# Kernel tuning notes

Measured on AMD Instinct MI355X. Metric: run time of the kernel, lower is better.

The kernel has to match this reference:

```python
import jax, jax.numpy as jnp
import numpy as np

E = 512   # embed_size == hidden_size (required: step-0 'embed' is the init output of size hidden)
H = 512
A = 512   # attention dim
V = 20000
P = 196
B = 128
T = 24


def setup_inputs() -> dict:
    key = jax.random.key(0)
    ks = jax.random.split(key, 20)
    s = 0.02
    return {
        "features": jax.random.normal(ks[0], (B, P, E), jnp.float32),
        "captions": jax.random.randint(ks[1], (B, T), 0, V),
        "emb": jax.random.normal(ks[2], (V, E), jnp.float32) * s,
        "W_init_h": jax.random.normal(ks[3], (E, H), jnp.float32) * s,
        "b_init_h": jnp.zeros((H,), jnp.float32),
        "W_init_o": jax.random.normal(ks[4], (E, H), jnp.float32) * s,
        "b_init_o": jnp.zeros((H,), jnp.float32),
        "Wf": jax.random.normal(ks[5], (E, A), jnp.float32) * s,
        "bf": jnp.zeros((A,), jnp.float32),
        "Wh": jax.random.normal(ks[6], (H, A), jnp.float32) * s,
        "bh": jnp.zeros((A,), jnp.float32),
        "v_att": jax.random.normal(ks[7], (A,), jnp.float32) * s,
        "W_ih": jax.random.normal(ks[8], (3 * H, 2 * E), jnp.float32) * s,
        "W_hh": jax.random.normal(ks[9], (3 * H, H), jnp.float32) * s,
        "b_ih": jnp.zeros((3 * H,), jnp.float32),
        "b_hh": jnp.zeros((3 * H,), jnp.float32),
        "W_out": jax.random.normal(ks[10], (V, H), jnp.float32) * s,
        "b_out": jnp.zeros((V,), jnp.float32),
    }


def reference(features, emb, W_init_h, b_init_h, W_init_o, b_init_o,
              Wf, bf, Wh, bh, v_att, W_ih, W_hh, b_ih, b_hh,
              W_out, b_out, captions):
    # init_hidden_state
    avg = features.mean(axis=1)                          # [B,E]
    hidden0 = jnp.tanh(avg @ W_init_h + b_init_h)        # [B,H]
    output0 = jnp.tanh(avg @ W_init_o + b_init_o)        # [B,H]

    emb_caps = emb[captions]                             # [B,T,E]
    # teacher forcing: step 0 uses init output, step i>0 uses embeddings[:, i-1]
    embed_seq = jnp.concatenate([output0[:, None, :], emb_caps[:, :-1, :]], axis=1)
    xs = embed_seq.transpose(1, 0, 2)                    # [T,B,E]

    feat_proj = features @ Wf + bf                       # [B,P,A] (precompute attn key proj)

    def step(h, x_emb):
        # additive attention over pixels
        score = jnp.tanh(feat_proj + (h @ Wh + bh)[:, None, :]) @ v_att   # [B,P]
        alpha = jax.nn.softmax(score, axis=1)
        ctx = jnp.einsum('bp,bpe->be', alpha, features)                   # [B,E]
        x = jnp.concatenate([x_emb, ctx], axis=1)                         # [B,2E]
        # single-step GRU (PyTorch gate order r,z,n)
        gi = x @ W_ih.T + b_ih
        gh = h @ W_hh.T + b_hh
        gi_r, gi_z, gi_n = jnp.split(gi, 3, axis=1)
        gh_r, gh_z, gh_n = jnp.split(gh, 3, axis=1)
        r = jax.nn.sigmoid(gi_r + gh_r)
        z = jax.nn.sigmoid(gi_z + gh_z)
        n = jnp.tanh(gi_n + r * gh_n)
        h_new = (1.0 - z) * n + z * h
        pred = h_new @ W_out.T + b_out                                    # [B,V]
        return h_new, pred

    _, preds = jax.lax.scan(step, hidden0, xs)           # preds: [T,B,V]
    return preds.transpose(1, 0, 2)                      # [B,T,V]
```

## Files before the change

kernel.cpp:

```cpp
#include <hip/hip_runtime.h>

#define Bb 128
#define Tt 24
#define Ee 512
#define Hh 512
#define Aa 512
#define Vv 20000
#define Pp 196
#define TV (Tt*Vv)
#define NBLK 512
#define NTHR 256
#define GT (NBLK*NTHR)
#define SMEM_BYTES 34816

typedef __attribute__((ext_vector_type(8))) short bfrag;
typedef __attribute__((ext_vector_type(4))) float f4;
typedef __attribute__((ext_vector_type(4))) unsigned short us4;

#define MFMA16(a,b,c) __builtin_amdgcn_mfma_f32_16x16x32_bf16(a,b,c,0,0,0)

__device__ __forceinline__ unsigned short f2bf(float f){
  unsigned int x = __builtin_bit_cast(unsigned int, f);
  x += 0x7fffu + ((x >> 16) & 1u);
  return (unsigned short)(x >> 16);
}
__device__ __forceinline__ float bfu2f(unsigned short u){
  unsigned int x = ((unsigned int)u) << 16;
  return __builtin_bit_cast(float, x);
}
#define LOG2E 1.442695041f
__device__ __forceinline__ float fexp2(float x){ return __builtin_amdgcn_exp2f(x); }
__device__ __forceinline__ float frcp (float x){ return __builtin_amdgcn_rcpf(x); }
__device__ __forceinline__ float tanh_f(float x){ return 1.0f - 2.0f*frcp(1.0f + fexp2((2.0f*LOG2E)*x)); }
__device__ __forceinline__ float sigm_f(float x){ return frcp(1.0f + fexp2(-LOG2E*x)); }

__device__ __forceinline__ unsigned long long scld8(const void* p){
  return __hip_atomic_load((const unsigned long long*)p, __ATOMIC_RELAXED, __HIP_MEMORY_SCOPE_AGENT);
}
__device__ __forceinline__ unsigned scld4(const unsigned* p){
  return __hip_atomic_load(p, __ATOMIC_RELAXED, __HIP_MEMORY_SCOPE_AGENT);
}
__device__ __forceinline__ void scst4(unsigned* p, unsigned v){
  __hip_atomic_store(p, v, __ATOMIC_RELAXED, __HIP_MEMORY_SCOPE_AGENT);
}
__device__ __forceinline__ void scstf(float* p, float v){
  __hip_atomic_store(p, v, __ATOMIC_RELAXED, __HIP_MEMORY_SCOPE_AGENT);
}

__device__ __forceinline__ void set_flag(unsigned* line, unsigned v){
  asm volatile("s_waitcnt vmcnt(0)" ::: "memory");
  __syncthreads();
  if(threadIdx.x == 0) scst4(line, v);
}
__device__ __forceinline__ void poll_flags(const unsigned* base, int n, unsigned tgt){
  int tid = threadIdx.x;
  for(;;){
    int ok = (tid < n) ? (scld4(base + tid*16) >= tgt) : 1;
    if(__syncthreads_count(ok) == NTHR) break;
    __builtin_amdgcn_s_sleep(4);
  }
  asm volatile("" ::: "memory");
}

__device__ __forceinline__ void gbar2(unsigned* sync, unsigned phase){
  __syncthreads();
  int tid = threadIdx.x, blk = blockIdx.x;
  if(tid == 0)
    (void)__hip_atomic_fetch_add(sync + (blk & 31)*16, 1u,
                                 __ATOMIC_RELEASE, __HIP_MEMORY_SCOPE_AGENT);
  if(blk == 0){
    for(;;){
      int ok = (tid < 32) ? (scld4(sync + tid*16) >= phase*16u) : 1;
      if(__syncthreads_count(ok) == NTHR) break;
      __builtin_amdgcn_s_sleep(2);
    }
    if(tid == 0) scst4(sync + 32*16, phase);
  }
  if(tid == 0){
    while(scld4(sync + 32*16) < phase) __builtin_amdgcn_s_sleep(2);
    (void)__hip_atomic_load(sync + 32*16, __ATOMIC_ACQUIRE, __HIP_MEMORY_SCOPE_AGENT);
  }
  __syncthreads();
}

__global__ void k_zero(unsigned* s){
  int i = blockIdx.x*256 + threadIdx.x;
  s[i] = 0u;
}

__device__ __forceinline__ void cast_loop(const float* __restrict__ s,
                                          unsigned short* __restrict__ d,
                                          int n4, int gtid){
  for(int i = gtid; i < n4; i += GT){
    float4 v = ((const float4*)s)[i];
    us4 o; o[0]=f2bf(v.x); o[1]=f2bf(v.y); o[2]=f2bf(v.z); o[3]=f2bf(v.w);
    ((us4*)d)[i] = o;
  }
}
__device__ __forceinline__ void tr_tile(const float* __restrict__ S,
                                        unsigned short* __restrict__ D,
                                        int it, int jt, int tid, float (*T)[33]){
  int er = tid>>3, c4 = (tid&7)*4;
  float4 v = *(const float4*)(S + (size_t)(jt*32+er)*512 + it*32 + c4);
  T[er][c4+0]=v.x; T[er][c4+1]=v.y; T[er][c4+2]=v.z; T[er][c4+3]=v.w;
  __syncthreads();
  us4 o;
  o[0]=f2bf(T[c4+0][er]); o[1]=f2bf(T[c4+1][er]);
  o[2]=f2bf(T[c4+2][er]); o[3]=f2bf(T[c4+3][er]);
  *(us4*)(D + (size_t)(it*32+er)*512 + jt*32 + c4) = o;
  __syncthreads();
}

__device__ __forceinline__ void stage16(char* dstSM, const unsigned short* src, int R0){
  int tid = threadIdx.x;
  #pragma unroll
  for(int j=0;j<8;j++){
    int u = tid + j*256;
    int row = u >> 7, c8 = u & 127;
    unsigned long long q = scld8(src + (size_t)(R0+row)*Hh + c8*4);
    int bo = (row<<10) + (c8<<3);
    bo ^= (row&7)<<4;
    *(unsigned long long*)(dstSM + bo) = q;
  }
}


__device__ void attention_task(int b, const float* __restrict__ hpr_t,
                               const unsigned short* __restrict__ fpb,
                               const unsigned short* __restrict__ featsB,
                               const float* __restrict__ vatt,
                               unsigned short* __restrict__ ctx_t, char* SM)
{
  float* hp  = (float*)SM;
  float* vp  = hp + 512;
  float* sc  = vp + 512;
  float* red = sc + 200;
  int tid = threadIdx.x;
  {
    unsigned long long q = scld8(hpr_t + (size_t)b*Aa + tid*2);
    float2 hv = __builtin_bit_cast(float2, q);
    float2 vv = *(const float2*)(vatt + tid*2);
    int a0 = tid*2, a1 = a0+1;
    hp[((a0&31)<<4)+(a0>>5)] = hv.x;
    hp[((a1&31)<<4)+(a1>>5)] = hv.y;
    vp[((a0&31)<<4)+(a0>>5)] = vv.x;
    vp[((a1&31)<<4)+(a1>>5)] = vv.y;
  }
  __syncthreads();
  int grp = tid >> 4, gl = tid & 15;
  for(int pass=0; pass<13; pass++){
    int p = pass*16 + grp;
    float acc = 0.0f;
    if(p < Pp){
      const unsigned short* fr = fpb + ((size_t)b*Pp + p)*Aa + gl*32;
      #pragma unroll
      for(int j=0;j<32;j+=8){
        bfrag fv = *(const bfrag*)(fr + j);
        #pragma unroll
        for(int q=0;q<8;q++){
          int idx = ((j+q)<<4) + gl;
          float x = bfu2f((unsigned short)fv[q]) + hp[idx];
          acc += tanh_f(x) * vp[idx];
        }
      }
    }
    acc += __shfl_xor(acc, 1, 64);
    acc += __shfl_xor(acc, 2, 64);
    acc += __shfl_xor(acc, 4, 64);
    acc += __shfl_xor(acc, 8, 64);
    if(p < Pp && gl == 0) sc[p] = acc;
  }
  __syncthreads();
  if(tid < 64){
    float m = -1e30f;
    for(int i=0;i<4;i++){ int p = tid + i*64; if(p < Pp) m = fmaxf(m, sc[p]); }
    for(int off=1; off<64; off<<=1) m = fmaxf(m, __shfl_xor(m, off, 64));
    float s = 0.0f;
    for(int i=0;i<4;i++){ int p = tid + i*64; if(p < Pp) s += fexp2((sc[p]-m)*LOG2E); }
    for(int off=1; off<64; off<<=1) s += __shfl_xor(s, off, 64);
    if(tid == 0){ red[0] = m; red[1] = frcp(s); }
  }
  __syncthreads();
  float mx = red[0], rS = red[1];
  float al_t = 0.0f;
  if(tid < Pp) al_t = fexp2((sc[tid]-mx)*LOG2E) * rS;
  __syncthreads();
  if(tid < Pp) sc[tid] = al_t;
  __syncthreads();
  float c0 = 0.f, c1 = 0.f;
  const unsigned int* fb = (const unsigned int*)(featsB + (size_t)b*Pp*Ee);
  for(int p=0;p<Pp;p++){
    float al = sc[p];
    unsigned int u = fb[(size_t)p*256 + tid];
    unsigned int lo = (u & 0xffffu) << 16, hi = u & 0xffff0000u;
    c0 += al * __builtin_bit_cast(float, lo);
    c1 += al * __builtin_bit_cast(float, hi);
  }
  unsigned int cw = ((unsigned int)f2bf(c1) << 16) | (unsigned int)f2bf(c0);
  scst4((unsigned*)ctx_t + (size_t)b*256 + tid, cw);
}

__device__ void hproj_mfma(int R0, int HC0, const char* SMh,
                           const unsigned short* __restrict__ WhT,
                           const float* __restrict__ bhv, float* __restrict__ hpr)
{
  int tid = threadIdx.x;
  int w = tid>>6, l = tid&63, l16 = l&15, lk = l>>4;
  int a = HC0 + w*16 + l16;
  f4 acc = (f4)(0.0f);
  for(int k0=0;k0<512;k0+=32){
    int koff = k0 + lk*8;
    int bo = (l16<<10) + (koff<<1); bo ^= (l16&7)<<4;
    bfrag ah = *(const bfrag*)(SMh + bo);
    bfrag bq = *(const bfrag*)(WhT + (size_t)a*Hh + koff);
    acc = MFMA16(ah, bq, acc);
  }
  float bias = bhv[a];
  #pragma unroll
  for(int i=0;i<4;i++){
    int row = lk*4 + i;
    scstf(hpr + (size_t)(R0+row)*Aa + a, acc[i] + bias);
  }
}

__device__ void gates_phaseA(int R0, int HC0, const unsigned short* __restrict__ eseqT,
                             const unsigned short* __restrict__ WihB,
                             const unsigned short* __restrict__ WhhB,
                             const char* SMh, f4 (&agh)[3], f4 (&agi)[3])
{
  int tid = threadIdx.x;
  int w = tid>>6, l = tid&63, l16 = l&15, lk = l>>4;
  int hcol = HC0 + w*16 + l16;
  #pragma unroll
  for(int q=0;q<3;q++){ agh[q]=(f4)(0.f); agi[q]=(f4)(0.f); }
  for(int k0=0;k0<512;k0+=32){
    int koff = k0 + lk*8;
    int bo = (l16<<10) + (koff<<1); bo ^= (l16&7)<<4;
    bfrag ah = *(const bfrag*)(SMh + bo);
    bfrag ae = *(const bfrag*)(eseqT + (size_t)(R0+l16)*Ee + koff);
    #pragma unroll
    for(int q=0;q<3;q++){
      int j = q*512 + hcol;
      bfrag bh_ = *(const bfrag*)(WhhB + (size_t)j*512  + koff);
      bfrag be  = *(const bfrag*)(WihB + (size_t)j*1024 + koff);
      agh[q] = MFMA16(ah, bh_, agh[q]);
      agi[q] = MFMA16(ae, be,  agi[q]);
    }
  }
}

__device__ void gates_phaseB(int R0, int HC0, const char* SMc,
                             const unsigned short* __restrict__ WihB,
                             const float* __restrict__ bih, const float* __restrict__ bhh,
                             const float* __restrict__ hf_cur, float* __restrict__ hf_nxt,
                             unsigned short* __restrict__ hbU_nxt,
                             f4 (&agh)[3], f4 (&agi)[3], char* SM_HB)
{
  int tid = threadIdx.x;
  int w = tid>>6, l = tid&63, l16 = l&15, lk = l>>4;
  int hcol = HC0 + w*16 + l16;
  for(int k0=0;k0<512;k0+=32){
    int koff = k0 + lk*8;
    int bo = (l16<<10) + (koff<<1); bo ^= (l16&7)<<4;
    bfrag ac = *(const bfrag*)(SMc + bo);
    #pragma unroll
    for(int q=0;q<3;q++){
      int j = q*512 + hcol;
      bfrag bc = *(const bfrag*)(WihB + (size_t)j*1024 + 512 + koff);
      agi[q] = MFMA16(ac, bc, agi[q]);
    }
  }
  float bir = bih[hcol],      bhr = bhh[hcol];
  float biz = bih[512+hcol],  bhz = bhh[512+hcol];
  float bin = bih[1024+hcol], bhn = bhh[1024+hcol];
  unsigned short (*HB)[64] = (unsigned short(*)[64])SM_HB;
  #pragma unroll
  for(int i=0;i<4;i++){
    int row = lk*4 + i;
    int b = R0 + row;
    float r_ = sigm_f(agi[0][i] + bir + agh[0][i] + bhr);
    float z_ = sigm_f(agi[1][i] + biz + agh[1][i] + bhz);
    float n_ = tanh_f(agi[2][i] + bin + r_*(agh[2][i] + bhn));
    float ho = hf_cur[(size_t)b*Hh + hcol];
    float hn = (1.0f - z_)*n_ + z_*ho;
    hf_nxt[(size_t)b*Hh + hcol] = hn;
    HB[row][w*16 + l16] = f2bf(hn);
  }
  __syncthreads();
  #pragma unroll
  for(int j=0;j<2;j++){
    int widx = tid + j*256;
    int row = widx >> 5, pr = widx & 31;
    unsigned uu = (unsigned)HB[row][pr*2] | ((unsigned)HB[row][pr*2+1] << 16);
    scst4((unsigned*)(hbU_nxt + (size_t)(R0+row)*Hh + HC0) + pr, uu);
  }
}

__device__ void pred_task32(int pt, int tw, const unsigned short* __restrict__ hb_cur,
                            const unsigned short* __restrict__ WoutB,
                            const float* __restrict__ bout, float* __restrict__ out,
                            char* SM)
{
  int tid = threadIdx.x;
  int vchunk = pt >> 2, mbase = (pt & 3)*32;
  #pragma unroll
  for(int j=0;j<16;j++){
    int u = tid + j*256;
    int row = u >> 7, c8 = u & 127;
    unsigned long long q = scld8(hb_cur + (size_t)(mbase+row)*Hh + c8*4);
    int bo = (row<<10) + (c8<<3);
    bo ^= (row&7)<<4;
    *(unsigned long long*)(SM + bo) = q;
  }
  __syncthreads();
  int w = tid>>6, l = tid&63, l16 = l&15, lk = l>>4;
  int nb = vchunk*256 + w*64;
  f4 acc[2][4];
  #pragma unroll
  for(int mi=0;mi<2;mi++) for(int ni=0;ni<4;ni++) acc[mi][ni] = (f4)(0.0f);
  for(int k0=0;k0<512;k0+=32){
    int koff = k0 + lk*8;
    bfrag af[2], bq[4];
    #pragma unroll
    for(int mi=0;mi<2;mi++){
      int row = mi*16 + l16;
      int bo = (row<<10) + (koff<<1);
      bo ^= (row&7)<<4;
      af[mi] = *(const bfrag*)(SM + bo);
    }
    #pragma unroll
    for(int ni=0;ni<4;ni++){
      int v = nb + ni*16 + l16; if(v > Vv-1) v = Vv-1;
      bq[ni] = *(const bfrag*)(WoutB + (size_t)v*Hh + koff);
    }
    #pragma unroll
    for(int mi=0;mi<2;mi++)
      #pragma unroll
      for(int ni=0;ni<4;ni++)
        acc[mi][ni] = MFMA16(af[mi], bq[ni], acc[mi][ni]);
  }
  #pragma unroll
  for(int ni=0;ni<4;ni++){
    int v = nb + ni*16 + l16;
    if(v < Vv){
      float bias = bout[v];
      #pragma unroll
      for(int mi=0;mi<2;mi++){
        #pragma unroll
        for(int i=0;i<4;i++){
          int br = mbase + mi*16 + lk*4 + i;
          __builtin_nontemporal_store(acc[mi][ni][i] + bias,
              out + (size_t)br*TV + (size_t)tw*Vv + v);
        }
      }
    }
  }
  __syncthreads();
}

__global__ __launch_bounds__(NTHR, 4) void k_all(
    const float* feats, const int* caps, const float* emb,
    const float* Winh, const float* binh, const float* Wino, const float* bino,
    const float* Wf, const float* bfv, const float* Wh, const float* bhv,
    const float* vatt, const float* Wih, const float* Whh,
    const float* bih, const float* bhh, const float* Wout, const float* bout,
    float* out,
    float* hfR, unsigned short* hbU, float* hpr,
    unsigned short* ctxR, unsigned short* avgB, unsigned short* eseq,
    unsigned short* WfT, unsigned short* WhT,
    unsigned short* WinhT, unsigned short* WinoT,
    unsigned short* WihB, unsigned short* WhhB,
    unsigned short* fpb, unsigned short* featsB, unsigned short* WoutB,
    unsigned* sync)
{
  extern __shared__ char SMEM[];
  const int blk = blockIdx.x, tid = threadIdx.x;
  const int gtid = blk*NTHR + tid;
  unsigned* flagsA = sync + 40*16;
  unsigned* flagsG = sync + 168*16;
  unsigned* flagsP = sync + 240*16;
  unsigned* aggP   = sync + 304*16;
  float* h_f0 = hfR;
  unsigned short* h_b0 = hbU;

  cast_loop(Wih,  WihB,  (3*Hh*2*Ee)/4, gtid);
  cast_loop(Whh,  WhhB,  (3*Hh*Hh)/4,   gtid);
  cast_loop(Wout, WoutB, (Vv*Hh)/4,     gtid);
  cast_loop(feats,featsB,(Bb*Pp*Ee)/4,  gtid);
  for(int task = blk; task < 1024; task += NBLK){
    int z = task >> 8, rt = task & 255;
    int it = rt & 15, jt = rt >> 4;
    const float* S = (z==0)?Wf:(z==1)?Wh:(z==2)?Winh:Wino;
    unsigned short* D = (z==0)?WfT:(z==1)?WhT:(z==2)?WinhT:WinoT;
    tr_tile(S, D, it, jt, tid, (float(*)[33])SMEM);
  }
  if(blk < Bb){
    int b = blk;
    const float* fb = feats + (size_t)b*Pp*Ee;
    float a0=0.f, a1=0.f;
    for(int p=0;p<Pp;p++){
      float2 v = *(const float2*)(fb + (size_t)p*Ee + tid*2);
      a0 += v.x; a1 += v.y;
    }
    a0 *= (1.0f/Pp); a1 *= (1.0f/Pp);
    unsigned int pack = ((unsigned int)f2bf(a1)<<16) | (unsigned int)f2bf(a0);
    ((unsigned int*)avgB)[(size_t)b*256 + tid] = pack;
  }
  for(int task = blk; task < (Tt-1)*Bb; task += NBLK){
    int ts = task/Bb + 1, b = task%Bb;
    int cap = caps[b*Tt + (ts-1)];
    float2 v = *(const float2*)(emb + (size_t)cap*Ee + tid*2);
    unsigned int pack = ((unsigned int)f2bf(v.y)<<16) | (unsigned int)f2bf(v.x);
    ((unsigned int*)(eseq + ((size_t)ts*Bb + b)*Ee))[tid] = pack;
  }
  gbar2(sync, 1);

  for(int task = blk; task < 1584; task += NBLK){
    int w = tid>>6, l = tid&63, l16 = l&15, lk = l>>4;
    if(task < 1568){
      int bx = task % 196, by = task / 196;
      size_t m_base = (size_t)bx*128 + (w&1)*64;
      int nb = by*64 + (w>>1)*32;
      f4 acc[4][2];
      #pragma unroll
      for(int mi=0;mi<4;mi++) for(int ni=0;ni<2;ni++) acc[mi][ni] = (f4)(0.0f);
      for(int k0=0;k0<512;k0+=32){
        int koff = k0 + lk*8;
        bfrag af[4], bq[2];
        #pragma unroll
        for(int mi=0;mi<4;mi++) af[mi] = *(const bfrag*)(featsB + (m_base+mi*16+l16)*512 + koff);
        #pragma unroll
        for(int ni=0;ni<2;ni++) bq[ni] = *(const bfrag*)(WfT + (size_t)(nb+ni*16+l16)*512 + koff);
        #pragma unroll
        for(int mi=0;mi<4;mi++)
          #pragma unroll
          for(int ni=0;ni<2;ni++)
            acc[mi][ni] = MFMA16(af[mi], bq[ni], acc[mi][ni]);
      }
      #pragma unroll
      for(int ni=0;ni<2;ni++){
        int a = nb + ni*16 + l16;
        float bias = bfv[a];
        #pragma unroll
        for(int mi=0;mi<4;mi++){
          size_t r = m_base + mi*16 + lk*4;
          #pragma unroll
          for(int i=0;i<4;i++)
            fpb[(r+i)*512 + a] = f2bf(acc[mi][ni][i] + bias);
        }
      }
    } else {
      int idx = task - 1568;
      int y = idx >> 3, xb = idx & 7;
      int m0 = (w&1)*64, nb = xb*64 + (w>>1)*32;
      const unsigned short* Wt = y ? WinoT : WinhT;
      const float* bias = y ? bino : binh;
      f4 acc[4][2];
      #pragma unroll
      for(int mi=0;mi<4;mi++) for(int ni=0;ni<2;ni++) acc[mi][ni] = (f4)(0.0f);
      for(int k0=0;k0<512;k0+=32){
        int koff = k0 + lk*8;
        bfrag af[4], bq[2];
        #pragma unroll
        for(int mi=0;mi<4;mi++) af[mi] = *(const bfrag*)(avgB + (size_t)(m0+mi*16+l16)*512 + koff);
        #pragma unroll
        for(int ni=0;ni<2;ni++) bq[ni] = *(const bfrag*)(Wt + (size_t)(nb+ni*16+l16)*512 + koff);
        #pragma unroll
        for(int mi=0;mi<4;mi++)
          #pragma unroll
          for(int ni=0;ni<2;ni++)
            acc[mi][ni] = MFMA16(af[mi], bq[ni], acc[mi][ni]);
      }
      #pragma unroll
      for(int ni=0;ni<2;ni++){
        int n = nb + ni*16 + l16;
        float bv = bias[n];
        #pragma unroll
        for(int mi=0;mi<4;mi++){
          int bb = m0 + mi*16 + lk*4;
          #pragma unroll
          for(int i=0;i<4;i++){
            float val = tanh_f(acc[mi][ni][i] + bv);
            if(y==0){ h_f0[(size_t)(bb+i)*Hh + n] = val; h_b0[(size_t)(bb+i)*Hh + n] = f2bf(val); }
            else    { eseq[(size_t)(bb+i)*Ee + n] = f2bf(val); }
          }
        }
      }
    }
  }
  gbar2(sync, 2);

  int xcd = blk & 7, slot = blk >> 3;

  if(slot < 16){
    int b = slot*8 + xcd;
    int rg = b >> 4;
    for(int t=0; t<Tt; t++){
      poll_flags(flagsP + rg*8*16, 8, (unsigned)(t+1));
      attention_task(b, hpr + (size_t)(t&1)*Bb*Aa, fpb, featsB, vatt,
                     ctxR + (size_t)(t&3)*Bb*Ee, SMEM);
      set_flag(flagsA + b*16, (unsigned)(t+1));
    }
  } else if(slot < 24){
    int r = slot - 16, c = xcd;
    int R0 = r*16, HC0 = c*64;
    char* SMh = SMEM;
    char* SMc = SMEM + 16384;
    char* SMB = SMEM + 32768;
    f4 agh[3], agi[3];
    stage16(SMh, hbU, R0);
    __syncthreads();
    hproj_mfma(R0, HC0, SMh, WhT, bhv, hpr);
    set_flag(flagsP + (r*8+c)*16, 1u);
    gates_phaseA(R0, HC0, eseq, WihB, WhhB, SMh, agh, agi);
    for(int t=0; t<Tt; t++){
      poll_flags(flagsA + R0*16, 16, (unsigned)(t+1));
      stage16(SMc, ctxR + (size_t)(t&3)*Bb*Ee, R0);
      __syncthreads();
      gates_phaseB(R0, HC0, SMc, WihB, bih, bhh,
                   hfR + (size_t)(t&1)*Bb*Hh, hfR + (size_t)((t+1)&1)*Bb*Hh,
                   hbU + (size_t)(t+1)*Bb*Hh, agh, agi, SMB);
      set_flag(flagsG + (r*8+c)*16, (unsigned)(t+1));
      if(t+1 < Tt){
        poll_flags(flagsG + r*8*16, 8, (unsigned)(t+1));
        stage16(SMh, hbU + (size_t)(t+1)*Bb*Hh, R0);
        __syncthreads();
        hproj_mfma(R0, HC0, SMh, WhT, bhv, hpr + (size_t)((t+1)&1)*Bb*Aa);
        set_flag(flagsP + (r*8+c)*16, (unsigned)(t+2));
        gates_phaseA(R0, HC0, eseq + (size_t)(t+1)*Bb*Ee, WihB, WhhB, SMh, agh, agi);
      }
    }
  } else {
    int ps = slot - 24;
    int pt = xcd*40 + ps;
    if(ps == 0){
      for(int t=1; t<=Tt; t++){
        poll_flags(flagsG, 64, (unsigned)t);
        if(tid == 0) scst4(aggP + xcd*16, (unsigned)t);
        pred_task32(pt, t-1, hbU + (size_t)t*Bb*Hh, WoutB, bout, out, SMEM);
      }
    } else if(pt < 316){
      for(int t=1; t<=Tt; t++){
        poll_flags(aggP + xcd*16, 1, (unsigned)t);
        pred_task32(pt, t-1, hbU + (size_t)t*Bb*Hh, WoutB, bout, out, SMEM);
      }
    }
  }
}

extern "C" void kernel_launch(void* const* d_in, const int* in_sizes, int n_in,
                              void* d_out, int out_size, void* d_ws, size_t ws_size,
                              hipStream_t stream)
{
  const float* feats = (const float*)d_in[0];
  const int*   caps  = (const int*)d_in[1];
  const float* emb   = (const float*)d_in[2];
  const float* Winh  = (const float*)d_in[3];
  const float* binh  = (const float*)d_in[4];
  const float* Wino  = (const float*)d_in[5];
  const float* bino  = (const float*)d_in[6];
  const float* Wf    = (const float*)d_in[7];
  const float* bfv   = (const float*)d_in[8];
  const float* Wh    = (const float*)d_in[9];
  const float* bhv   = (const float*)d_in[10];
  const float* vatt  = (const float*)d_in[11];
  const float* Wih   = (const float*)d_in[12];
  const float* Whh   = (const float*)d_in[13];
  const float* bih   = (const float*)d_in[14];
  const float* bhh   = (const float*)d_in[15];
  const float* Wout  = (const float*)d_in[16];
  const float* bout  = (const float*)d_in[17];
  float* out = (float*)d_out;

  char* ws = (char*)d_ws;
  size_t off = 0;
  auto alloc = [&](size_t bytes){
    off = (off + 255) & ~(size_t)255;
    void* p = ws + off; off += bytes; return p;
  };
  unsigned* syncp = (unsigned*)alloc(32768);
  float* hfR = (float*)alloc((size_t)2*Bb*Hh*4);
  unsigned short* hbU = (unsigned short*)alloc((size_t)(Tt+1)*Bb*Hh*2);
  float* hpr = (float*)alloc((size_t)2*Bb*Aa*4);
  unsigned short* ctxR  = (unsigned short*)alloc((size_t)4*Bb*Ee*2);
  unsigned short* avgB  = (unsigned short*)alloc((size_t)Bb*Ee*2);
  unsigned short* eseq  = (unsigned short*)alloc((size_t)Tt*Bb*Ee*2);
  unsigned short* WfT   = (unsigned short*)alloc((size_t)Ee*Aa*2);
  unsigned short* WhT   = (unsigned short*)alloc((size_t)Hh*Aa*2);
  unsigned short* WinhT = (unsigned short*)alloc((size_t)Ee*Hh*2);
  unsigned short* WinoT = (unsigned short*)alloc((size_t)Ee*Hh*2);
  unsigned short* WihB  = (unsigned short*)alloc((size_t)3*Hh*2*Ee*2);
  unsigned short* WhhB  = (unsigned short*)alloc((size_t)3*Hh*Hh*2);
  unsigned short* fpb   = (unsigned short*)alloc((size_t)Bb*Pp*Aa*2);
  unsigned short* featsB= (unsigned short*)alloc((size_t)Bb*Pp*Ee*2);
  unsigned short* WoutB = (unsigned short*)alloc((size_t)Vv*Hh*2);
  if(ws_size < off) return;

  k_zero<<<32, 256, 0, stream>>>(syncp);
  k_all<<<NBLK, NTHR, SMEM_BYTES, stream>>>(
      feats, caps, emb, Winh, binh, Wino, bino, Wf, bfv, Wh, bhv, vatt,
      Wih, Whh, bih, bhh, Wout, bout, out,
      hfR, hbU, hpr, ctxR, avgB, eseq,
      WfT, WhT, WinhT, WinoT, WihB, WhhB, fpb, featsB, WoutB, syncp);
}
```

Baseline: 1.445 ms.

## Batch output projection over two timesteps to reuse W_out loads

The prediction blocks now wait for two consecutive hidden states and run the vocabulary projection for both together, so each W_out fragment loaded from memory feeds twice as many MFMAs. Shared memory grows to 64KB and launch bounds drop to 2 blocks per CU to fit the second staged hidden tile. The gate scratch buffer is padded to a stride of 88, the context loop is unrolled, and the poll sleep is shortened. In exchange, predictions lag the recurrence by an extra step, and the lower occupancy bound may raise register use or limit co-residency of the 512 persistent blocks.

Measured after the change: 1.448 ms. About the same (+0.2%).

```diff
diff --git a/kernel.cpp b/kernel.cpp
--- a/kernel.cpp
+++ b/kernel.cpp
@@ -11,7 +11,7 @@
 #define NBLK 512
 #define NTHR 256
 #define GT (NBLK*NTHR)
-#define SMEM_BYTES 34816
+#define SMEM_BYTES 65536
 
 typedef __attribute__((ext_vector_type(8))) short bfrag;
 typedef __attribute__((ext_vector_type(4))) float f4;
@@ -57,7 +57,7 @@
   for(;;){
     int ok = (tid < n) ? (scld4(base + tid*16) >= tgt) : 1;
     if(__syncthreads_count(ok) == NTHR) break;
-    __builtin_amdgcn_s_sleep(4);
+    __builtin_amdgcn_s_sleep(2);
   }
   asm volatile("" ::: "memory");
 }
@@ -189,6 +189,7 @@
   __syncthreads();
   float c0 = 0.f, c1 = 0.f;
   const unsigned int* fb = (const unsigned int*)(featsB + (size_t)b*Pp*Ee);
+  #pragma unroll 4
   for(int p=0;p<Pp;p++){
     float al = sc[p];
     unsigned int u = fb[(size_t)p*256 + tid];
@@ -240,9 +241,9 @@
     bfrag ae = *(const bfrag*)(eseqT + (size_t)(R0+l16)*Ee + koff);
     #pragma unroll
     for(int q=0;q<3;q++){
-      int j = q*512 + hcol;
-      bfrag bh_ = *(const bfrag*)(WhhB + (size_t)j*512  + koff);
-      bfrag be  = *(const bfrag*)(WihB + (size_t)j*1024 + koff);
+      int jj = q*512 + hcol;
+      bfrag bh_ = *(const bfrag*)(WhhB + (size_t)jj*512  + koff);
+      bfrag be  = *(const bfrag*)(WihB + (size_t)jj*1024 + koff);
       agh[q] = MFMA16(ah, bh_, agh[q]);
       agi[q] = MFMA16(ae, be,  agi[q]);
     }
@@ -254,7 +255,7 @@
                              const float* __restrict__ bih, const float* __restrict__ bhh,
                              const float* __restrict__ hf_cur, float* __restrict__ hf_nxt,
                              unsigned short* __restrict__ hbU_nxt,
-                             f4 (&agh)[3], f4 (&agi)[3], char* SM_HB)
+                             f4 (&agh)[3], f4 (&agi)[3], unsigned short* HBp)
 {
   int tid = threadIdx.x;
   int w = tid>>6, l = tid&63, l16 = l&15, lk = l>>4;
@@ -265,15 +266,14 @@
     bfrag ac = *(const bfrag*)(SMc + bo);
     #pragma unroll
     for(int q=0;q<3;q++){
-      int j = q*512 + hcol;
-      bfrag bc = *(const bfrag*)(WihB + (size_t)j*1024 + 512 + koff);
+      int jj = q*512 + hcol;
+      bfrag bc = *(const bfrag*)(WihB + (size_t)jj*1024 + 512 + koff);
       agi[q] = MFMA16(ac, bc, agi[q]);
     }
   }
   float bir = bih[hcol],      bhr = bhh[hcol];
   float biz = bih[512+hcol],  bhz = bhh[512+hcol];
   float bin = bih[1024+hcol], bhn = bhh[1024+hcol];
-  unsigned short (*HB)[64] = (unsigned short(*)[64])SM_HB;
   #pragma unroll
   for(int i=0;i<4;i++){
     int row = lk*4 + i;
@@ -284,22 +284,24 @@
     float ho = hf_cur[(size_t)b*Hh + hcol];
     float hn = (1.0f - z_)*n_ + z_*ho;
     hf_nxt[(size_t)b*Hh + hcol] = hn;
-    HB[row][w*16 + l16] = f2bf(hn);
+    HBp[row*88 + w*16 + l16] = f2bf(hn);
   }
   __syncthreads();
   #pragma unroll
   for(int j=0;j<2;j++){
     int widx = tid + j*256;
     int row = widx >> 5, pr = widx & 31;
-    unsigned uu = (unsigned)HB[row][pr*2] | ((unsigned)HB[row][pr*2+1] << 16);
+    unsigned uu = (unsigned)HBp[row*88 + pr*2] | ((unsigned)HBp[row*88 + pr*2+1] << 16);
     scst4((unsigned*)(hbU_nxt + (size_t)(R0+row)*Hh + HC0) + pr, uu);
   }
 }
 
-__device__ void pred_task32(int pt, int tw, const unsigned short* __restrict__ hb_cur,
-                            const unsigned short* __restrict__ WoutB,
-                            const float* __restrict__ bout, float* __restrict__ out,
-                            char* SM)
+__device__ void pred_pair(int pt, int twA,
+                          const unsigned short* __restrict__ hbA,
+                          const unsigned short* __restrict__ hbB,
+                          const unsigned short* __restrict__ WoutB,
+                          const float* __restrict__ bout, float* __restrict__ out,
+                          char* SM)
 {
   int tid = threadIdx.x;
   int vchunk = pt >> 2, mbase = (pt & 3)*32;
@@ -307,26 +309,29 @@
   for(int j=0;j<16;j++){
     int u = tid + j*256;
     int row = u >> 7, c8 = u & 127;
-    unsigned long long q = scld8(hb_cur + (size_t)(mbase+row)*Hh + c8*4);
+    unsigned long long qa = scld8(hbA + (size_t)(mbase+row)*Hh + c8*4);
+    unsigned long long qb = scld8(hbB + (size_t)(mbase+row)*Hh + c8*4);
     int bo = (row<<10) + (c8<<3);
     bo ^= (row&7)<<4;
-    *(unsigned long long*)(SM + bo) = q;
+    *(unsigned long long*)(SM + bo) = qa;
+    *(unsigned long long*)(SM + 32768 + bo) = qb;
   }
   __syncthreads();
   int w = tid>>6, l = tid&63, l16 = l&15, lk = l>>4;
   int nb = vchunk*256 + w*64;
-  f4 acc[2][4];
-  #pragma unroll
-  for(int mi=0;mi<2;mi++) for(int ni=0;ni<4;ni++) acc[mi][ni] = (f4)(0.0f);
+  f4 accA[2][4], accB[2][4];
+  #pragma unroll
+  for(int mi=0;mi<2;mi++) for(int ni=0;ni<4;ni++){ accA[mi][ni]=(f4)(0.0f); accB[mi][ni]=(f4)(0.0f); }
   for(int k0=0;k0<512;k0+=32){
     int koff = k0 + lk*8;
-    bfrag af[2], bq[4];
+    bfrag afA[2], afB[2], bq[4];
     #pragma unroll
     for(int mi=0;mi<2;mi++){
       int row = mi*16 + l16;
       int bo = (row<<10) + (koff<<1);
       bo ^= (row&7)<<4;
-      af[mi] = *(const bfrag*)(SM + bo);
+      afA[mi] = *(const bfrag*)(SM + bo);
+      afB[mi] = *(const bfrag*)(SM + 32768 + bo);
     }
     #pragma unroll
     for(int ni=0;ni<4;ni++){
@@ -336,8 +341,10 @@
     #pragma unroll
     for(int mi=0;mi<2;mi++)
       #pragma unroll
-      for(int ni=0;ni<4;ni++)
-        acc[mi][ni] = MFMA16(af[mi], bq[ni], acc[mi][ni]);
+      for(int ni=0;ni<4;ni++){
+        accA[mi][ni] = MFMA16(afA[mi], bq[ni], accA[mi][ni]);
+        accB[mi][ni] = MFMA16(afB[mi], bq[ni], accB[mi][ni]);
+      }
   }
   #pragma unroll
   for(int ni=0;ni<4;ni++){
@@ -349,8 +356,10 @@
         #pragma unroll
         for(int i=0;i<4;i++){
           int br = mbase + mi*16 + lk*4 + i;
-          __builtin_nontemporal_store(acc[mi][ni][i] + bias,
-              out + (size_t)br*TV + (size_t)tw*Vv + v);
+          __builtin_nontemporal_store(accA[mi][ni][i] + bias,
+              out + (size_t)br*TV + (size_t)twA*Vv + v);
+          __builtin_nontemporal_store(accB[mi][ni][i] + bias,
+              out + (size_t)br*TV + (size_t)(twA+1)*Vv + v);
         }
       }
     }
@@ -358,7 +367,7 @@
   __syncthreads();
 }
 
-__global__ __launch_bounds__(NTHR, 4) void k_all(
+__global__ __launch_bounds__(NTHR, 2) void k_all(
     const float* feats, const int* caps, const float* emb,
     const float* Winh, const float* binh, const float* Wino, const float* bino,
     const float* Wf, const float* bfv, const float* Wh, const float* bhv,
@@ -506,7 +515,7 @@
     int R0 = r*16, HC0 = c*64;
     char* SMh = SMEM;
     char* SMc = SMEM + 16384;
-    char* SMB = SMEM + 32768;
+    unsigned short* HBp = (unsigned short*)(SMEM + 32768);
     f4 agh[3], agi[3];
     stage16(SMh, hbU, R0);
     __syncthreads();
@@ -519,7 +528,7 @@
       __syncthreads();
       gates_phaseB(R0, HC0, SMc, WihB, bih, bhh,
                    hfR + (size_t)(t&1)*Bb*Hh, hfR + (size_t)((t+1)&1)*Bb*Hh,
-                   hbU + (size_t)(t+1)*Bb*Hh, agh, agi, SMB);
+                   hbU + (size_t)(t+1)*Bb*Hh, agh, agi, HBp);
       set_flag(flagsG + (r*8+c)*16, (unsigned)(t+1));
       if(t+1 < Tt){
         poll_flags(flagsG + r*8*16, 8, (unsigned)(t+1));
@@ -534,15 +543,19 @@
     int ps = slot - 24;
     int pt = xcd*40 + ps;
     if(ps == 0){
-      for(int t=1; t<=Tt; t++){
-        poll_flags(flagsG, 64, (unsigned)t);
-        if(tid == 0) scst4(aggP + xcd*16, (unsigned)t);
-        pred_task32(pt, t-1, hbU + (size_t)t*Bb*Hh, WoutB, bout, out, SMEM);
+      for(int pp=0; pp<12; pp++){
+        int t1 = 2*pp + 2;
+        poll_flags(flagsG, 64, (unsigned)t1);
+        if(tid == 0) scst4(aggP + xcd*16, (unsigned)t1);
+        pred_pair(pt, 2*pp, hbU + (size_t)(2*pp+1)*Bb*Hh,
+                  hbU + (size_t)(2*pp+2)*Bb*Hh, WoutB, bout, out, SMEM);
       }
     } else if(pt < 316){
-      for(int t=1; t<=Tt; t++){
-        poll_flags(aggP + xcd*16, 1, (unsigned)t);
-        pred_task32(pt, t-1, hbU + (size_t)t*Bb*Hh, WoutB, bout, out, SMEM);
+      for(int pp=0; pp<12; pp++){
+        int t1 = 2*pp + 2;
+        poll_flags(aggP + xcd*16, 1, (unsigned)t1);
+        pred_pair(pt, 2*pp, hbU + (size_t)(2*pp+1)*Bb*Hh,
+                  hbU + (size_t)(2*pp+2)*Bb*Hh, WoutB, bout, out, SMEM);
       }
     }
   }
```
